# Kernel tuning notes

Measured on AMD Instinct MI355X. Metric: run time of the kernel, lower is better.

## Reference

```python
import jax, jax.numpy as jnp
import numpy as np

NEG_INF = -1e9  # stands in for the -inf diagonal mask of criss-cross attention
BN_EPS = 1e-5


def conv1x1(x, w, b=None):
    # x: [B,Cin,H,W], w: [Cout,Cin]
    y = jnp.einsum('bchw,oc->bohw', x, w)
    if b is not None:
        y = y + b[None, :, None, None]
    return y


def criss_cross(qf, kf, vf, q_w, q_b, k_w, k_b, v_w, v_b, gamma):
    # Criss-cross attention (CCNet): row + column affinity, joint softmax, aggregate.
    B, C, H, W = vf.shape
    q = conv1x1(qf, q_w, q_b)  # [B,Ci,H,W]
    k = conv1x1(kf, k_w, k_b)  # [B,Ci,H,W]
    v = conv1x1(vf, v_w, v_b)  # [B,C,H,W]
    # column-wise (along H) energy, with -inf on the self position (h == h')
    eH = jnp.einsum('bchw,bcHw->bhwH', q, k)
    eH = eH + NEG_INF * jnp.eye(H, dtype=eH.dtype)[:, None, :]  # [H,1,H] broadcasts over w
    # row-wise (along W) energy
    eW = jnp.einsum('bchw,bchW->bhwW', q, k)
    att = jax.nn.softmax(jnp.concatenate([eH, eW], axis=-1), axis=-1)  # [B,H,W,H+W]
    aH, aW = att[..., :H], att[..., H:]
    outH = jnp.einsum('bcHw,bhwH->bchw', v, aH)
    outW = jnp.einsum('bchW,bhwW->bchw', v, aW)
    return gamma * (outH + outW) + vf


def batchnorm(x, scale, bias):
    # training-mode BN over (N,H,W)
    mean = x.mean(axis=(0, 2, 3), keepdims=True)
    var = x.var(axis=(0, 2, 3), keepdims=True)
    xh = (x - mean) * jax.lax.rsqrt(var + BN_EPS)
    return xh * scale[None, :, None, None] + bias[None, :, None, None]


def setup_inputs() -> dict:
    key = jax.random.key(0)
    ks = jax.random.split(key, 16)
    B, C, H, W = 8, 512, 96, 96
    Hh, Wh = 48, 48
    Cin = C // 2    # 256
    Ci = C // 16    # 32
    s = 0.02
    inp = {
        'low_feature': jax.random.normal(ks[0], (B, C, H, W), jnp.float32),
        'high_feature': jax.random.normal(ks[1], (B, C, Hh, Wh), jnp.float32),
        'conv1_w': jax.random.normal(ks[2], (Cin, C), jnp.float32) * s,
        'conv1_b': jnp.zeros((Cin,), jnp.float32),
        'conv2_w': jax.random.normal(ks[3], (Cin, C), jnp.float32) * s,
        'conv2_b': jnp.zeros((Cin,), jnp.float32),
        'q_w': jax.random.normal(ks[4], (Ci, Cin), jnp.float32) * s,
        'q_b': jnp.zeros((Ci,), jnp.float32),
        'k_w': jax.random.normal(ks[5], (Ci, Cin), jnp.float32) * s,
        'k_b': jnp.zeros((Ci,), jnp.float32),
        'v_w': jax.random.normal(ks[6], (Cin, Cin), jnp.float32) * s,
        'v_b': jnp.zeros((Cin,), jnp.float32),
        'gamma': jnp.array(0.1, jnp.float32),
        'bottleneck_w': jax.random.normal(ks[7], (C, Cin + C), jnp.float32) * s,
        'bn_scale': jnp.ones((C,), jnp.float32),
        'bn_bias': jnp.zeros((C,), jnp.float32),
    }
    return inp


def reference(low_feature, high_feature, conv1_w, conv1_b, conv2_w, conv2_b,
              q_w, q_b, k_w, k_b, v_w, v_b, gamma, bottleneck_w, bn_scale, bn_bias):
    B, C, H, W = low_feature.shape
    hf = jax.image.resize(high_feature, (B, high_feature.shape[1], H, W), method='bilinear')
    qf = conv1x1(low_feature, conv1_w, conv1_b)   # [B,C/2,H,W]
    vf = conv1x1(hf, conv2_w, conv2_b)            # [B,C/2,H,W]
    for _ in range(2):  # module applies the same attention twice
        vf = criss_cross(qf, vf, vf, q_w, q_b, k_w, k_b, v_w, v_b, gamma)
    cat = jnp.concatenate([vf, hf], axis=1)       # [B, C/2 + C, H, W]
    out = conv1x1(cat, bottleneck_w)              # bias=False
    out = batchnorm(out, bn_scale, bn_bias)
    return jax.nn.relu(out)
```

## Files before the change

### kernel.cpp

```cpp
#include <hip/hip_runtime.h>
#include <hip/hip_bf16.h>

typedef __hip_bfloat16 bf16;
typedef __attribute__((ext_vector_type(8))) short short8;
typedef __attribute__((ext_vector_type(4))) float f32x4;

constexpr int kHW = 96 * 96;

__device__ __forceinline__ float b2f(bf16 x){ return __bfloat162float(x); }
__device__ __forceinline__ bf16  f2b(float x){ return __float2bfloat16(x); }
__device__ __forceinline__ unsigned short b2u(bf16 x){ return *(unsigned short*)&x; }


__global__ void k_zero(float* __restrict__ p){
  int i = blockIdx.x*256 + threadIdx.x;
  if (i < 1024) p[i] = 0.0f;
}

__global__ void k_cvt(const float* __restrict__ s, bf16* __restrict__ d, int n){
  int i = blockIdx.x*256 + threadIdx.x;
  if (i < n) d[i] = f2b(s[i]);
}

__global__ __launch_bounds__(256) void k_upsample(const float* __restrict__ hi,
                                                  bf16* __restrict__ hf_t){
  int y = blockIdx.x, b = blockIdx.y, t = threadIdx.x;
  int j = y >> 1;
  int j0, j1; float wy0, wy1;
  if ((y & 1) == 0){ j0 = j - 1; if (j0 < 0) j0 = 0; j1 = j; wy0 = 0.25f; wy1 = 0.75f; }
  else             { j0 = j; j1 = j + 1; if (j1 > 47) j1 = 47; wy0 = 0.75f; wy1 = 0.25f; }
  __shared__ __align__(16) float sm[2][128][49];
  for (int c0 = 0; c0 < 512; c0 += 128){
    for (int e = t; e < 2*128*48; e += 256){
      int cl = e / 96; int r = e % 96; int jj = r / 48; int i = r % 48;
      int row = jj ? j1 : j0;
      sm[jj][cl][i] = hi[(((size_t)b*512 + c0 + cl)*48 + row)*48 + i];
    }
    __syncthreads();
    for (int e = t; e < 96*128; e += 256){
      int x = e >> 7; int cl = e & 127;
      int i = x >> 1; int i0, i1; float wx0, wx1;
      if ((x & 1) == 0){ i0 = i - 1; if (i0 < 0) i0 = 0; i1 = i; wx0 = 0.25f; wx1 = 0.75f; }
      else             { i0 = i; i1 = i + 1; if (i1 > 47) i1 = 47; wx0 = 0.75f; wx1 = 0.25f; }
      float v = wy0*(wx0*sm[0][cl][i0] + wx1*sm[0][cl][i1])
              + wy1*(wx0*sm[1][cl][i0] + wx1*sm[1][cl][i1]);
      hf_t[(((size_t)b*96 + x)*96 + y)*512 + c0 + cl] = f2b(v);
    }
    __syncthreads();
  }
}

__global__ void k_qqw(const float* __restrict__ q_w, const float* __restrict__ c1_w,
                      bf16* __restrict__ qq_wb){
  int gid = blockIdx.x*256 + threadIdx.x;
  int o = gid >> 9, c = gid & 511;
  float acc = 0.f;
  for (int k = 0; k < 256; k++) acc += q_w[o*256 + k] * c1_w[k*512 + c];
  qq_wb[gid] = f2b(acc);
}
__global__ void k_qqb(const float* __restrict__ q_w, const float* __restrict__ c1_b,
                      const float* __restrict__ q_b, float* __restrict__ qq_b){
  int o = threadIdx.x; if (o >= 32) return;
  float acc = q_b[o];
  for (int k = 0; k < 256; k++) acc += q_w[o*256 + k] * c1_b[k];
  qq_b[o] = acc;
}

__global__ __launch_bounds__(256) void k_mfma_gemm(const bf16* __restrict__ A,
                                                   const bf16* __restrict__ Wb,
                                                   const float* __restrict__ bias,
                                                   bf16* __restrict__ out,
                                                   int K, int O){
  int b = blockIdx.z, n0 = blockIdx.x*128, o0 = blockIdx.y*128;
  int t = threadIdx.x, lane = t & 63, wv = t >> 6;
  int m_off = (wv & 1)*64, o_off = (wv >> 1)*64;
  int lm = lane & 15, lk = lane >> 4;
  __shared__ __align__(16) bf16 As[2][128*40];
  __shared__ __align__(16) bf16 Ws[2][128*40];
  f32x4 acc[4][4] = {};
  const bf16* Ab = A + (size_t)b*kHW*K;
  int nl0 = t >> 2, p0 = (t & 3)*8;
  uint4 pa0, pa1, pw0, pw1;
  pa0 = *(const uint4*)&Ab[(size_t)(n0+nl0)*K + p0];
  pa1 = *(const uint4*)&Ab[(size_t)(n0+nl0+64)*K + p0];
  pw0 = *(const uint4*)&Wb[(size_t)(o0+nl0)*K + p0];
  pw1 = *(const uint4*)&Wb[(size_t)(o0+nl0+64)*K + p0];
  *(uint4*)&As[0][nl0*40 + p0]      = pa0;
  *(uint4*)&As[0][(nl0+64)*40 + p0] = pa1;
  *(uint4*)&Ws[0][nl0*40 + p0]      = pw0;
  *(uint4*)&Ws[0][(nl0+64)*40 + p0] = pw1;
  int cur = 0;
  int NS = K >> 5;
  for (int s = 0; s < NS; s++){
    if (s+1 < NS){
      int c0 = (s+1)*32;
      pa0 = *(const uint4*)&Ab[(size_t)(n0+nl0)*K + c0 + p0];
      pa1 = *(const uint4*)&Ab[(size_t)(n0+nl0+64)*K + c0 + p0];
      pw0 = *(const uint4*)&Wb[(size_t)(o0+nl0)*K + c0 + p0];
      pw1 = *(const uint4*)&Wb[(size_t)(o0+nl0+64)*K + c0 + p0];
    }
    __syncthreads();
    short8 af[4], bfr[4];
    #pragma unroll
    for (int i = 0; i < 4; i++){
      af[i]  = *(const short8*)&As[cur][(m_off + i*16 + lm)*40 + lk*8];
      bfr[i] = *(const short8*)&Ws[cur][(o_off + i*16 + lm)*40 + lk*8];
    }
    #pragma unroll
    for (int i = 0; i < 4; i++)
      #pragma unroll
      for (int j = 0; j < 4; j++)
        acc[i][j] = __builtin_amdgcn_mfma_f32_16x16x32_bf16(af[i], bfr[j], acc[i][j], 0, 0, 0);
    if (s+1 < NS){
      int nx = cur ^ 1;
      *(uint4*)&As[nx][nl0*40 + p0]      = pa0;
      *(uint4*)&As[nx][(nl0+64)*40 + p0] = pa1;
      *(uint4*)&Ws[nx][nl0*40 + p0]      = pw0;
      *(uint4*)&Ws[nx][(nl0+64)*40 + p0] = pw1;
      cur = nx;
    }
  }
  #pragma unroll
  for (int j = 0; j < 4; j++){
    int oc = o0 + o_off + j*16 + lm;
    float bs = bias ? bias[oc] : 0.0f;
    #pragma unroll
    for (int i = 0; i < 4; i++){
      int rbase = n0 + m_off + i*16 + lk*4;
      #pragma unroll
      for (int r = 0; r < 4; r++)
        out[((size_t)b*kHW + rbase + r)*(size_t)O + oc] = f2b(acc[i][j][r] + bs);
    }
  }
}

__global__ __launch_bounds__(256) void k_bneck_mfma(const bf16* __restrict__ vf,
                                                    const bf16* __restrict__ hf,
                                                    const bf16* __restrict__ Wb,
                                                    bf16* __restrict__ out,
                                                    float* __restrict__ s1,
                                                    float* __restrict__ s2){
  int b = blockIdx.z, n0 = blockIdx.x*128, o0 = blockIdx.y*128;
  int t = threadIdx.x, lane = t & 63, wv = t >> 6;
  int m_off = (wv & 1)*64, o_off = (wv >> 1)*64;
  int lm = lane & 15, lk = lane >> 4;
  __shared__ __align__(16) bf16 As[2][128*40];
  __shared__ __align__(16) bf16 Ws[2][128*40];
  __shared__ float l1[128];
  __shared__ float l2[128];
  if (t < 128){ l1[t] = 0.f; l2[t] = 0.f; }
  f32x4 acc[4][4] = {};
  int nl0 = t >> 2, p0 = (t & 3)*8;
  const bf16* vfb = vf + (size_t)b*kHW*256;
  const bf16* hfb = hf + (size_t)b*kHW*512;
  uint4 pa0, pa1, pw0, pw1;
  pa0 = *(const uint4*)&vfb[(size_t)(n0+nl0)*256 + p0];
  pa1 = *(const uint4*)&vfb[(size_t)(n0+nl0+64)*256 + p0];
  pw0 = *(const uint4*)&Wb[(size_t)(o0+nl0)*768 + p0];
  pw1 = *(const uint4*)&Wb[(size_t)(o0+nl0+64)*768 + p0];
  *(uint4*)&As[0][nl0*40 + p0]      = pa0;
  *(uint4*)&As[0][(nl0+64)*40 + p0] = pa1;
  *(uint4*)&Ws[0][nl0*40 + p0]      = pw0;
  *(uint4*)&Ws[0][(nl0+64)*40 + p0] = pw1;
  int cur = 0;
  for (int s = 0; s < 24; s++){
    if (s+1 < 24){
      int c0 = (s+1)*32;
      if (c0 < 256){
        pa0 = *(const uint4*)&vfb[(size_t)(n0+nl0)*256 + c0 + p0];
        pa1 = *(const uint4*)&vfb[(size_t)(n0+nl0+64)*256 + c0 + p0];
      } else {
        int cc = c0 - 256;
        pa0 = *(const uint4*)&hfb[(size_t)(n0+nl0)*512 + cc + p0];
        pa1 = *(const uint4*)&hfb[(size_t)(n0+nl0+64)*512 + cc + p0];
      }
      pw0 = *(const uint4*)&Wb[(size_t)(o0+nl0)*768 + c0 + p0];
      pw1 = *(const uint4*)&Wb[(size_t)(o0+nl0+64)*768 + c0 + p0];
    }
    __syncthreads();
    short8 af[4], bfr[4];
    #pragma unroll
    for (int i = 0; i < 4; i++){
      af[i]  = *(const short8*)&As[cur][(m_off + i*16 + lm)*40 + lk*8];
      bfr[i] = *(const short8*)&Ws[cur][(o_off + i*16 + lm)*40 + lk*8];
    }
    #pragma unroll
    for (int i = 0; i < 4; i++)
      #pragma unroll
      for (int j = 0; j < 4; j++)
        acc[i][j] = __builtin_amdgcn_mfma_f32_16x16x32_bf16(af[i], bfr[j], acc[i][j], 0, 0, 0);
    if (s+1 < 24){
      int nx = cur ^ 1;
      *(uint4*)&As[nx][nl0*40 + p0]      = pa0;
      *(uint4*)&As[nx][(nl0+64)*40 + p0] = pa1;
      *(uint4*)&Ws[nx][nl0*40 + p0]      = pw0;
      *(uint4*)&Ws[nx][(nl0+64)*40 + p0] = pw1;
      cur = nx;
    }
  }
  #pragma unroll
  for (int j = 0; j < 4; j++){
    int oc = o0 + o_off + j*16 + lm;
    float p1 = 0.f, p2 = 0.f;
    #pragma unroll
    for (int i = 0; i < 4; i++){
      int rbase = n0 + m_off + i*16 + lk*4;
      #pragma unroll
      for (int r = 0; r < 4; r++){
        float v = acc[i][j][r];
        p1 += v; p2 += v*v;
        out[((size_t)b*kHW + rbase + r)*512 + oc] = f2b(v);
      }
    }
    int cl = o_off + j*16 + lm;
    atomicAdd(&l1[cl], p1);
    atomicAdd(&l2[cl], p2);
  }
  __syncthreads();
  if (t < 128){
    atomicAdd(&s1[o0 + t], l1[t]);
    atomicAdd(&s2[o0 + t], l2[t]);
  }
}

__global__ __launch_bounds__(256) void k_qmfma(const float* __restrict__ low,
                                               const bf16* __restrict__ qq_wb,
                                               const float* __restrict__ qq_b,
                                               bf16* __restrict__ q_t){
  int n0 = blockIdx.x*64, b = blockIdx.y, t = threadIdx.x;
  int lane = t & 63, wv = t >> 6;
  int m_off = wv*16;
  int lm = lane & 15, lk = lane >> 4;
  __shared__ __align__(16) bf16 As[64*36];
  __shared__ __align__(16) bf16 Ws[32*40];
  f32x4 acc[2] = {};
  const float* low_b = low + (size_t)b*512*kHW;
  int c2 = (t & 15)*2;
  int xg = t >> 4;
  for (int c0 = 0; c0 < 512; c0 += 32){
    const float* p0 = low_b + (size_t)(c0 + c2)*kHW + n0 + xg*4;
    float4 a0 = *(const float4*)p0;
    float4 a1 = *(const float4*)(p0 + kHW);
    float f0[4] = {a0.x, a0.y, a0.z, a0.w};
    float f1[4] = {a1.x, a1.y, a1.z, a1.w};
    #pragma unroll
    for (int u = 0; u < 4; u++){
      ushort2 pr;
      bf16 v0 = f2b(f0[u]), v1 = f2b(f1[u]);
      pr.x = b2u(v0); pr.y = b2u(v1);
      *(ushort2*)&As[(xg*4 + u)*36 + c2] = pr;
    }
    if (t < 128){
      int ol = t >> 2, p = t & 3;
      *(uint4*)&Ws[ol*40 + p*8] = *(const uint4*)&qq_wb[(size_t)ol*512 + c0 + p*8];
    }
    __syncthreads();
    short8 af = *(const short8*)&As[(m_off + lm)*36 + lk*8];
    short8 b0 = *(const short8*)&Ws[lm*40 + lk*8];
    short8 b1 = *(const short8*)&Ws[(16 + lm)*40 + lk*8];
    acc[0] = __builtin_amdgcn_mfma_f32_16x16x32_bf16(af, b0, acc[0], 0, 0, 0);
    acc[1] = __builtin_amdgcn_mfma_f32_16x16x32_bf16(af, b1, acc[1], 0, 0, 0);
    __syncthreads();
  }
  #pragma unroll
  for (int j = 0; j < 2; j++){
    int oc = j*16 + lm;
    float bs = qq_b[oc];
    #pragma unroll
    for (int r = 0; r < 4; r++){
      int ng = n0 + m_off + lk*4 + r;
      int h = ng / 96, x = ng - h*96;
      q_t[(((size_t)b*96 + x)*96 + h)*32 + oc] = f2b(acc[j][r] + bs);
    }
  }
}

template<int BN, int OT>
__global__ __launch_bounds__(256) void k_gemm_bb(const bf16* __restrict__ A,
                                                 const float* __restrict__ Wt,
                                                 const float* __restrict__ bias,
                                                 bf16* __restrict__ out,
                                                 int Cin, int O){
  constexpr int TN = BN/4;
  int b = blockIdx.z, n0 = blockIdx.x*BN, o0 = blockIdx.y*OT, t = threadIdx.x;
  int tn = t % TN, to = t / TN;
  __shared__ __align__(16) float As[32][BN+4];
  __shared__ __align__(16) float Ws[32][OT+4];
  float acc[4][4] = {};
  const bf16* Ab = A + (size_t)b*kHW*Cin;
  for (int c0 = 0; c0 < Cin; c0 += 32){
    for (int e = t; e < BN*32; e += 256){
      int nl = e >> 5, kk = e & 31;
      As[kk][nl] = b2f(Ab[(size_t)(n0+nl)*Cin + c0 + kk]);
    }
    for (int e = t; e < OT*32; e += 256){
      int ol = e >> 5, kk = e & 31;
      Ws[kk][ol] = Wt[(size_t)(o0+ol)*Cin + c0 + kk];
    }
    __syncthreads();
    #pragma unroll
    for (int kk = 0; kk < 32; kk++){
      float4 av = *(const float4*)&As[kk][tn*4];
      float4 wv = *(const float4*)&Ws[kk][to*4];
      float a_[4] = {av.x, av.y, av.z, av.w};
      float w_[4] = {wv.x, wv.y, wv.z, wv.w};
      #pragma unroll
      for (int i = 0; i < 4; i++)
        #pragma unroll
        for (int jj = 0; jj < 4; jj++) acc[i][jj] += a_[i]*w_[jj];
    }
    __syncthreads();
  }
  #pragma unroll
  for (int i = 0; i < 4; i++){
    size_t base = ((size_t)b*kHW + n0 + tn*4 + i)*(size_t)O + o0 + to*4;
    #pragma unroll
    for (int jj = 0; jj < 4; jj++) out[base + jj] = f2b(acc[i][jj] + bias[o0 + to*4 + jj]);
  }
}

__global__ __launch_bounds__(256) void k_eH(const bf16* __restrict__ q_t,
                                            const bf16* __restrict__ k_t,
                                            bf16* __restrict__ att){
  int w = blockIdx.x, b = blockIdx.y, t = threadIdx.x;
  __shared__ float Qs[96][33];
  __shared__ float Ks[96][33];
  const bf16* Qp = q_t + (((size_t)b*96 + w)*96)*32;
  const bf16* Kp = k_t + (((size_t)b*96 + w)*96)*32;
  for (int e = t; e < 3072; e += 256){ Qs[e>>5][e&31] = b2f(Qp[e]); Ks[e>>5][e&31] = b2f(Kp[e]); }
  __syncthreads();
  int tj = t % 16, th = t / 16;
  float acc[6][6] = {};
  #pragma unroll 4
  for (int c = 0; c < 32; c++){
    float qa[6], kb[6];
    #pragma unroll
    for (int i = 0; i < 6; i++) qa[i] = Qs[th*6 + i][c];
    #pragma unroll
    for (int jj = 0; jj < 6; jj++) kb[jj] = Ks[tj*6 + jj][c];
    #pragma unroll
    for (int i = 0; i < 6; i++)
      #pragma unroll
      for (int jj = 0; jj < 6; jj++) acc[i][jj] += qa[i]*kb[jj];
  }
  #pragma unroll
  for (int i = 0; i < 6; i++){
    int h = th*6 + i;
    size_t base = (((size_t)b*96 + h)*96 + w)*192;
    #pragma unroll
    for (int jj = 0; jj < 6; jj++){
      int jg = tj*6 + jj;
      float e = acc[i][jj];
      if (jg == h) e += -1000000000.0f;
      att[base + jg] = f2b(e);
    }
  }
}

__global__ __launch_bounds__(256) void k_eW(const bf16* __restrict__ q_t,
                                            const bf16* __restrict__ k_t,
                                            bf16* __restrict__ att){
  int h = blockIdx.x, b = blockIdx.y, t = threadIdx.x;
  __shared__ float Qs[96][33];
  __shared__ float Ks[96][33];
  for (int e = t; e < 3072; e += 256){
    int wl = e >> 5, c = e & 31;
    size_t idx = (((size_t)b*96 + wl)*96 + h)*32 + c;
    Qs[wl][c] = b2f(q_t[idx]);
    Ks[wl][c] = b2f(k_t[idx]);
  }
  __syncthreads();
  int tj = t % 16, tw = t / 16;
  float acc[6][6] = {};
  #pragma unroll 4
  for (int c = 0; c < 32; c++){
    float qa[6], kb[6];
    #pragma unroll
    for (int i = 0; i < 6; i++) qa[i] = Qs[tw*6 + i][c];
    #pragma unroll
    for (int jj = 0; jj < 6; jj++) kb[jj] = Ks[tj*6 + jj][c];
    #pragma unroll
    for (int i = 0; i < 6; i++)
      #pragma unroll
      for (int jj = 0; jj < 6; jj++) acc[i][jj] += qa[i]*kb[jj];
  }
  #pragma unroll
  for (int i = 0; i < 6; i++){
    int wl = tw*6 + i;
    size_t base = (((size_t)b*96 + h)*96 + wl)*192 + 96;
    #pragma unroll
    for (int jj = 0; jj < 6; jj++) att[base + tj*6 + jj] = f2b(acc[i][jj]);
  }
}

__global__ __launch_bounds__(256) void k_softmax(bf16* __restrict__ att){
  int t = threadIdx.x;
  int row = blockIdx.x*4 + (t >> 6);
  int lane = t & 63;
  size_t base = (size_t)row * 192;
  float x0 = b2f(att[base + lane]);
  float x1 = b2f(att[base + 64 + lane]);
  float x2 = b2f(att[base + 128 + lane]);
  float m = fmaxf(x0, fmaxf(x1, x2));
  #pragma unroll
  for (int off = 32; off; off >>= 1) m = fmaxf(m, __shfl_xor(m, off));
  float e0 = __expf(x0 - m), e1 = __expf(x1 - m), e2 = __expf(x2 - m);
  float s = e0 + e1 + e2;
  #pragma unroll
  for (int off = 32; off; off >>= 1) s += __shfl_xor(s, off);
  float inv = 1.0f / s;
  att[base + lane]       = f2b(e0 * inv);
  att[base + 64 + lane]  = f2b(e1 * inv);
  att[base + 128 + lane] = f2b(e2 * inv);
}

__global__ __launch_bounds__(256) void k_outH_mfma(const bf16* __restrict__ att,
                                                   const bf16* __restrict__ v_t,
                                                   bf16* __restrict__ accb){
  int w = blockIdx.x, b = blockIdx.y, t = threadIdx.x;
  int lane = t & 63, wv = t >> 6;
  int m_off = (wv & 1)*48, o_off = (wv >> 1)*128;
  int lm = lane & 15, lk = lane >> 4;
  __shared__ __align__(16) bf16 As[96*36];
  __shared__ __align__(16) bf16 Vt[256*36];
  f32x4 acc[3][8] = {};
  const bf16* Vb = v_t + ((size_t)b*96 + w)*96*256;
  for (int j0 = 0; j0 < 96; j0 += 32){
    for (int e = t; e < 384; e += 256){
      int h = e >> 2, p = e & 3;
      *(uint4*)&As[h*36 + p*8] =
        *(const uint4*)&att[(((size_t)b*96 + h)*96 + w)*192 + j0 + p*8];
    }
    for (int e = t; e < 512; e += 256){
      int jj2 = (e & 15)*2, cg = e >> 4;
      const bf16* p = Vb + (size_t)(j0 + jj2)*256 + cg*8;
      uint4 a0 = *(const uint4*)p;
      uint4 a1 = *(const uint4*)(p + 256);
      const unsigned short* u0 = (const unsigned short*)&a0;
      const unsigned short* u1 = (const unsigned short*)&a1;
      #pragma unroll
      for (int u = 0; u < 8; u++){
        ushort2 pr; pr.x = u0[u]; pr.y = u1[u];
        *(ushort2*)&Vt[(cg*8 + u)*36 + jj2] = pr;
      }
    }
    __syncthreads();
    short8 af[3], bfr[8];
    #pragma unroll
    for (int i = 0; i < 3; i++)
      af[i] = *(const short8*)&As[(m_off + i*16 + lm)*36 + lk*8];
    #pragma unroll
    for (int j = 0; j < 8; j++)
      bfr[j] = *(const short8*)&Vt[(o_off + j*16 + lm)*36 + lk*8];
    #pragma unroll
    for (int i = 0; i < 3; i++)
      #pragma unroll
      for (int j = 0; j < 8; j++)
        acc[i][j] = __builtin_amdgcn_mfma_f32_16x16x32_bf16(af[i], bfr[j], acc[i][j], 0, 0, 0);
    __syncthreads();
  }
  #pragma unroll
  for (int j = 0; j < 8; j++){
    int c = o_off + j*16 + lm;
    #pragma unroll
    for (int i = 0; i < 3; i++){
      int hbase = m_off + i*16 + lk*4;
      #pragma unroll
      for (int r = 0; r < 4; r++)
        accb[(((size_t)b*96 + w)*96 + hbase + r)*256 + c] = f2b(acc[i][j][r]);
    }
  }
}

__global__ __launch_bounds__(256) void k_outW_mfma(const bf16* __restrict__ att,
                                                   const bf16* __restrict__ v_t,
                                                   const bf16* __restrict__ accb,
                                                   const float* __restrict__ gamma_p,
                                                   bf16* __restrict__ vf_t){
  int h = blockIdx.x, b = blockIdx.y, t = threadIdx.x;
  int lane = t & 63, wv = t >> 6;
  int m_off = (wv & 1)*48, o_off = (wv >> 1)*128;
  int lm = lane & 15, lk = lane >> 4;
  __shared__ __align__(16) bf16 As[96*36];
  __shared__ __align__(16) bf16 Vt[256*36];
  f32x4 acc[3][8] = {};
  for (int j0 = 0; j0 < 96; j0 += 32){
    for (int e = t; e < 384; e += 256){
      int wl = e >> 2, p = e & 3;
      *(uint4*)&As[wl*36 + p*8] =
        *(const uint4*)&att[(((size_t)b*96 + h)*96 + wl)*192 + 96 + j0 + p*8];
    }
    for (int e = t; e < 512; e += 256){
      int jj2 = (e & 15)*2, cg = e >> 4;
      const bf16* p = v_t + (((size_t)b*96 + j0 + jj2)*96 + h)*256 + cg*8;
      uint4 a0 = *(const uint4*)p;
      uint4 a1 = *(const uint4*)(p + 96*256);
      const unsigned short* u0 = (const unsigned short*)&a0;
      const unsigned short* u1 = (const unsigned short*)&a1;
      #pragma unroll
      for (int u = 0; u < 8; u++){
        ushort2 pr; pr.x = u0[u]; pr.y = u1[u];
        *(ushort2*)&Vt[(cg*8 + u)*36 + jj2] = pr;
      }
    }
    __syncthreads();
    short8 af[3], bfr[8];
    #pragma unroll
    for (int i = 0; i < 3; i++)
      af[i] = *(const short8*)&As[(m_off + i*16 + lm)*36 + lk*8];
    #pragma unroll
    for (int j = 0; j < 8; j++)
      bfr[j] = *(const short8*)&Vt[(o_off + j*16 + lm)*36 + lk*8];
    #pragma unroll
    for (int i = 0; i < 3; i++)
      #pragma unroll
      for (int j = 0; j < 8; j++)
        acc[i][j] = __builtin_amdgcn_mfma_f32_16x16x32_bf16(af[i], bfr[j], acc[i][j], 0, 0, 0);
    __syncthreads();
  }
  float g = gamma_p[0];
  #pragma unroll
  for (int j = 0; j < 8; j++){
    int c = o_off + j*16 + lm;
    #pragma unroll
    for (int i = 0; i < 3; i++){
      int wbase = m_off + i*16 + lk*4;
      #pragma unroll
      for (int r = 0; r < 4; r++){
        size_t idx = (((size_t)b*96 + wbase + r)*96 + h)*256 + c;
        vf_t[idx] = f2b(b2f(vf_t[idx]) + g*(acc[i][j][r] + b2f(accb[idx])));
      }
    }
  }
}

__global__ void k_bnprep(const float* __restrict__ s1, const float* __restrict__ s2,
                         const float* __restrict__ sc, const float* __restrict__ bi,
                         float2* __restrict__ ab){
  int co = blockIdx.x*256 + threadIdx.x;
  if (co >= 512) return;
  const float N = 73728.0f;
  float mean = s1[co] / N;
  float var  = s2[co] / N - mean*mean;
  if (var < 0.f) var = 0.f;
  float a = rsqrtf(var + 1e-5f) * sc[co];
  ab[co] = make_float2(a, bi[co] - mean*a);
}

__global__ __launch_bounds__(256) void k_bnout(const bf16* __restrict__ bt,
                                               const float2* __restrict__ ab,
                                               float* __restrict__ out){
  int w0 = blockIdx.x*32, h = blockIdx.y, b = blockIdx.z, t = threadIdx.x;
  __shared__ float Tl[32][33];
  for (int co0 = 0; co0 < 512; co0 += 32){
    for (int e = t; e < 1024; e += 256){
      int wl = e >> 5, co = e & 31;
      Tl[wl][co] = b2f(bt[(((size_t)b*96 + w0 + wl)*96 + h)*512 + co0 + co]);
    }
    __syncthreads();
    for (int e = t; e < 1024; e += 256){
      int co = e >> 5, wl = e & 31;
      float2 s = ab[co0 + co];
      float v = fmaxf(Tl[wl][co]*s.x + s.y, 0.0f);
      out[(((size_t)b*512 + co0 + co)*96 + h)*96 + w0 + wl] = v;
    }
    __syncthreads();
  }
}

extern "C" void kernel_launch(void* const* d_in, const int* in_sizes, int n_in,
                              void* d_out, int out_size, void* d_ws, size_t ws_size,
                              hipStream_t stream){
  (void)in_sizes; (void)n_in; (void)out_size; (void)ws_size;
  const float* low   = (const float*)d_in[0];
  const float* high  = (const float*)d_in[1];
  const float* c1w   = (const float*)d_in[2];
  const float* c1b   = (const float*)d_in[3];
  const float* c2w   = (const float*)d_in[4];
  const float* c2b   = (const float*)d_in[5];
  const float* qw    = (const float*)d_in[6];
  const float* qb    = (const float*)d_in[7];
  const float* kw    = (const float*)d_in[8];
  const float* kb    = (const float*)d_in[9];
  const float* vw    = (const float*)d_in[10];
  const float* vb    = (const float*)d_in[11];
  const float* gamma = (const float*)d_in[12];
  const float* bw    = (const float*)d_in[13];
  const float* bns   = (const float*)d_in[14];
  const float* bnb   = (const float*)d_in[15];
  float* out = (float*)d_out;

  char* wsb = (char*)d_ws;
  bf16*   hf_t = (bf16*) (wsb + 0);
  bf16*   vf_t = (bf16*) (wsb + 75497472);
  bf16*   q_t  = (bf16*) (wsb + 113246208);
  bf16*   qq_wb= (bf16*) (wsb + 117964800);
  float*  qq_b = (float*)(wsb + 118030336);
  float*  s1   = (float*)(wsb + 118030464);
  float*  s2   = (float*)(wsb + 118032512);
  float2* ab   = (float2*)(wsb + 118034560);
  bf16*   wbb  = (bf16*) (wsb + 118038656);
  bf16*   wc2  = (bf16*) (wsb + 118825088);
  bf16*   wv   = (bf16*) (wsb + 119087232);
  bf16*   v_t  = (bf16*) (wsb + 119218304);
  bf16*   att  = (bf16*) (wsb + 156967040);
  bf16*   accb = (bf16*) (wsb + 185278592);
  bf16*   k_t  = (bf16*) (wsb + 185278592);
  bf16*   bt   = (bf16*) (wsb + 119218304);

  k_zero<<<4, 256, 0, stream>>>(s1);
  k_cvt<<<1536, 256, 0, stream>>>(bw,  wbb, 393216);
  k_cvt<<<512,  256, 0, stream>>>(c2w, wc2, 131072);
  k_cvt<<<256,  256, 0, stream>>>(vw,  wv,  65536);
  k_upsample<<<dim3(96, 8), 256, 0, stream>>>(high, hf_t);
  k_qqw<<<64, 256, 0, stream>>>(qw, c1w, qq_wb);
  k_qqb<<<1, 64, 0, stream>>>(qw, c1b, qb, qq_b);
  k_mfma_gemm<<<dim3(72, 2, 8), 256, 0, stream>>>(hf_t, wc2, c2b, vf_t, 512, 256);
  k_qmfma<<<dim3(144, 8), 256, 0, stream>>>(low, qq_wb, qq_b, q_t);

  for (int r = 0; r < 2; r++){
    k_gemm_bb<128, 32><<<dim3(72, 1, 8), 256, 0, stream>>>(vf_t, kw, kb, k_t, 256, 32);
    k_mfma_gemm<<<dim3(72, 2, 8), 256, 0, stream>>>(vf_t, wv, vb, v_t, 256, 256);
    k_eH<<<dim3(96, 8), 256, 0, stream>>>(q_t, k_t, att);
    k_eW<<<dim3(96, 8), 256, 0, stream>>>(q_t, k_t, att);
    k_softmax<<<18432, 256, 0, stream>>>(att);
    k_outH_mfma<<<dim3(96, 8), 256, 0, stream>>>(att, v_t, accb);
    k_outW_mfma<<<dim3(96, 8), 256, 0, stream>>>(att, v_t, accb, gamma, vf_t);
  }

  k_bneck_mfma<<<dim3(72, 4, 8), 256, 0, stream>>>(vf_t, hf_t, wbb, bt, s1, s2);
  k_bnprep<<<2, 256, 0, stream>>>(s1, s2, bns, bnb, ab);
  k_bnout<<<dim3(3, 96, 8), 256, 0, stream>>>(bt, ab, out);
}
```

Before: 1.014 ms.

## Use MFMA for key projection and XOR-swizzle shared tiles in GEMMs

```diff
diff --git a/kernel.cpp b/kernel.cpp
--- a/kernel.cpp
+++ b/kernel.cpp
@@ -10,6 +10,8 @@
 __device__ __forceinline__ float b2f(bf16 x){ return __bfloat162float(x); }
 __device__ __forceinline__ bf16  f2b(float x){ return __float2bfloat16(x); }
 __device__ __forceinline__ unsigned short b2u(bf16 x){ return *(unsigned short*)&x; }
+
+#define SW(r, g) ((r)*32 + ((((g) ^ (((r) >> 1) & 3))) << 3))
 
 
 __global__ void k_zero(float* __restrict__ p){
@@ -75,20 +77,20 @@
   int t = threadIdx.x, lane = t & 63, wv = t >> 6;
   int m_off = (wv & 1)*64, o_off = (wv >> 1)*64;
   int lm = lane & 15, lk = lane >> 4;
-  __shared__ __align__(16) bf16 As[2][128*40];
-  __shared__ __align__(16) bf16 Ws[2][128*40];
+  __shared__ __align__(16) bf16 As[2][128*32];
+  __shared__ __align__(16) bf16 Ws[2][128*32];
   f32x4 acc[4][4] = {};
   const bf16* Ab = A + (size_t)b*kHW*K;
-  int nl0 = t >> 2, p0 = (t & 3)*8;
+  int nl0 = t >> 2, gp = t & 3, p0 = gp*8;
   uint4 pa0, pa1, pw0, pw1;
   pa0 = *(const uint4*)&Ab[(size_t)(n0+nl0)*K + p0];
   pa1 = *(const uint4*)&Ab[(size_t)(n0+nl0+64)*K + p0];
   pw0 = *(const uint4*)&Wb[(size_t)(o0+nl0)*K + p0];
   pw1 = *(const uint4*)&Wb[(size_t)(o0+nl0+64)*K + p0];
-  *(uint4*)&As[0][nl0*40 + p0]      = pa0;
-  *(uint4*)&As[0][(nl0+64)*40 + p0] = pa1;
-  *(uint4*)&Ws[0][nl0*40 + p0]      = pw0;
-  *(uint4*)&Ws[0][(nl0+64)*40 + p0] = pw1;
+  *(uint4*)&As[0][SW(nl0, gp)]    = pa0;
+  *(uint4*)&As[0][SW(nl0+64, gp)] = pa1;
+  *(uint4*)&Ws[0][SW(nl0, gp)]    = pw0;
+  *(uint4*)&Ws[0][SW(nl0+64, gp)] = pw1;
   int cur = 0;
   int NS = K >> 5;
   for (int s = 0; s < NS; s++){
@@ -103,8 +105,8 @@
     short8 af[4], bfr[4];
     #pragma unroll
     for (int i = 0; i < 4; i++){
-      af[i]  = *(const short8*)&As[cur][(m_off + i*16 + lm)*40 + lk*8];
-      bfr[i] = *(const short8*)&Ws[cur][(o_off + i*16 + lm)*40 + lk*8];
+      af[i]  = *(const short8*)&As[cur][SW(m_off + i*16 + lm, lk)];
+      bfr[i] = *(const short8*)&Ws[cur][SW(o_off + i*16 + lm, lk)];
     }
     #pragma unroll
     for (int i = 0; i < 4; i++)
@@ -113,10 +115,10 @@
         acc[i][j] = __builtin_amdgcn_mfma_f32_16x16x32_bf16(af[i], bfr[j], acc[i][j], 0, 0, 0);
     if (s+1 < NS){
       int nx = cur ^ 1;
-      *(uint4*)&As[nx][nl0*40 + p0]      = pa0;
-      *(uint4*)&As[nx][(nl0+64)*40 + p0] = pa1;
-      *(uint4*)&Ws[nx][nl0*40 + p0]      = pw0;
-      *(uint4*)&Ws[nx][(nl0+64)*40 + p0] = pw1;
+      *(uint4*)&As[nx][SW(nl0, gp)]    = pa0;
+      *(uint4*)&As[nx][SW(nl0+64, gp)] = pa1;
+      *(uint4*)&Ws[nx][SW(nl0, gp)]    = pw0;
+      *(uint4*)&Ws[nx][SW(nl0+64, gp)] = pw1;
       cur = nx;
     }
   }
@@ -144,13 +146,13 @@
   int t = threadIdx.x, lane = t & 63, wv = t >> 6;
   int m_off = (wv & 1)*64, o_off = (wv >> 1)*64;
   int lm = lane & 15, lk = lane >> 4;
-  __shared__ __align__(16) bf16 As[2][128*40];
-  __shared__ __align__(16) bf16 Ws[2][128*40];
+  __shared__ __align__(16) bf16 As[2][128*32];
+  __shared__ __align__(16) bf16 Ws[2][128*32];
   __shared__ float l1[128];
   __shared__ float l2[128];
   if (t < 128){ l1[t] = 0.f; l2[t] = 0.f; }
   f32x4 acc[4][4] = {};
-  int nl0 = t >> 2, p0 = (t & 3)*8;
+  int nl0 = t >> 2, gp = t & 3, p0 = gp*8;
   const bf16* vfb = vf + (size_t)b*kHW*256;
   const bf16* hfb = hf + (size_t)b*kHW*512;
   uint4 pa0, pa1, pw0, pw1;
@@ -158,10 +160,10 @@
   pa1 = *(const uint4*)&vfb[(size_t)(n0+nl0+64)*256 + p0];
   pw0 = *(const uint4*)&Wb[(size_t)(o0+nl0)*768 + p0];
   pw1 = *(const uint4*)&Wb[(size_t)(o0+nl0+64)*768 + p0];
-  *(uint4*)&As[0][nl0*40 + p0]      = pa0;
-  *(uint4*)&As[0][(nl0+64)*40 + p0] = pa1;
-  *(uint4*)&Ws[0][nl0*40 + p0]      = pw0;
-  *(uint4*)&Ws[0][(nl0+64)*40 + p0] = pw1;
+  *(uint4*)&As[0][SW(nl0, gp)]    = pa0;
+  *(uint4*)&As[0][SW(nl0+64, gp)] = pa1;
+  *(uint4*)&Ws[0][SW(nl0, gp)]    = pw0;
+  *(uint4*)&Ws[0][SW(nl0+64, gp)] = pw1;
   int cur = 0;
   for (int s = 0; s < 24; s++){
     if (s+1 < 24){
@@ -181,8 +183,8 @@
     short8 af[4], bfr[4];
     #pragma unroll
     for (int i = 0; i < 4; i++){
-      af[i]  = *(const short8*)&As[cur][(m_off + i*16 + lm)*40 + lk*8];
-      bfr[i] = *(const short8*)&Ws[cur][(o_off + i*16 + lm)*40 + lk*8];
+      af[i]  = *(const short8*)&As[cur][SW(m_off + i*16 + lm, lk)];
+      bfr[i] = *(const short8*)&Ws[cur][SW(o_off + i*16 + lm, lk)];
     }
     #pragma unroll
     for (int i = 0; i < 4; i++)
@@ -191,10 +193,10 @@
         acc[i][j] = __builtin_amdgcn_mfma_f32_16x16x32_bf16(af[i], bfr[j], acc[i][j], 0, 0, 0);
     if (s+1 < 24){
       int nx = cur ^ 1;
-      *(uint4*)&As[nx][nl0*40 + p0]      = pa0;
-      *(uint4*)&As[nx][(nl0+64)*40 + p0] = pa1;
-      *(uint4*)&Ws[nx][nl0*40 + p0]      = pw0;
-      *(uint4*)&Ws[nx][(nl0+64)*40 + p0] = pw1;
+      *(uint4*)&As[nx][SW(nl0, gp)]    = pa0;
+      *(uint4*)&As[nx][SW(nl0+64, gp)] = pa1;
+      *(uint4*)&Ws[nx][SW(nl0, gp)]    = pw0;
+      *(uint4*)&Ws[nx][SW(nl0+64, gp)] = pw1;
       cur = nx;
     }
   }
@@ -275,47 +277,67 @@
   }
 }
 
-template<int BN, int OT>
-__global__ __launch_bounds__(256) void k_gemm_bb(const bf16* __restrict__ A,
-                                                 const float* __restrict__ Wt,
-                                                 const float* __restrict__ bias,
-                                                 bf16* __restrict__ out,
-                                                 int Cin, int O){
-  constexpr int TN = BN/4;
-  int b = blockIdx.z, n0 = blockIdx.x*BN, o0 = blockIdx.y*OT, t = threadIdx.x;
-  int tn = t % TN, to = t / TN;
-  __shared__ __align__(16) float As[32][BN+4];
-  __shared__ __align__(16) float Ws[32][OT+4];
-  float acc[4][4] = {};
-  const bf16* Ab = A + (size_t)b*kHW*Cin;
-  for (int c0 = 0; c0 < Cin; c0 += 32){
-    for (int e = t; e < BN*32; e += 256){
-      int nl = e >> 5, kk = e & 31;
-      As[kk][nl] = b2f(Ab[(size_t)(n0+nl)*Cin + c0 + kk]);
-    }
-    for (int e = t; e < OT*32; e += 256){
-      int ol = e >> 5, kk = e & 31;
-      Ws[kk][ol] = Wt[(size_t)(o0+ol)*Cin + c0 + kk];
-    }
-    __syncthreads();
-    #pragma unroll
-    for (int kk = 0; kk < 32; kk++){
-      float4 av = *(const float4*)&As[kk][tn*4];
-      float4 wv = *(const float4*)&Ws[kk][to*4];
-      float a_[4] = {av.x, av.y, av.z, av.w};
-      float w_[4] = {wv.x, wv.y, wv.z, wv.w};
-      #pragma unroll
-      for (int i = 0; i < 4; i++)
-        #pragma unroll
-        for (int jj = 0; jj < 4; jj++) acc[i][jj] += a_[i]*w_[jj];
-    }
-    __syncthreads();
-  }
-  #pragma unroll
-  for (int i = 0; i < 4; i++){
-    size_t base = ((size_t)b*kHW + n0 + tn*4 + i)*(size_t)O + o0 + to*4;
-    #pragma unroll
-    for (int jj = 0; jj < 4; jj++) out[base + jj] = f2b(acc[i][jj] + bias[o0 + to*4 + jj]);
+__global__ __launch_bounds__(256) void k_kmfma(const bf16* __restrict__ A,
+                                               const bf16* __restrict__ Wk,
+                                               const float* __restrict__ bias,
+                                               bf16* __restrict__ out){
+  int n0 = blockIdx.x*128, b = blockIdx.y;
+  int t = threadIdx.x, lane = t & 63, wv = t >> 6;
+  int m_off = wv*32;
+  int lm = lane & 15, lk = lane >> 4;
+  __shared__ __align__(16) bf16 As[2][128*32];
+  __shared__ __align__(16) bf16 Ws[2][32*32];
+  f32x4 acc[2][2] = {};
+  const bf16* Ab = A + (size_t)b*kHW*256;
+  int nl0 = t >> 2, gp = t & 3, p0 = gp*8;
+  int ol = t >> 2;
+  uint4 pa0, pa1, pw;
+  pa0 = *(const uint4*)&Ab[(size_t)(n0+nl0)*256 + p0];
+  pa1 = *(const uint4*)&Ab[(size_t)(n0+nl0+64)*256 + p0];
+  if (t < 128) pw = *(const uint4*)&Wk[(size_t)ol*256 + p0];
+  *(uint4*)&As[0][SW(nl0, gp)]    = pa0;
+  *(uint4*)&As[0][SW(nl0+64, gp)] = pa1;
+  if (t < 128) *(uint4*)&Ws[0][SW(ol, gp)] = pw;
+  int cur = 0;
+  for (int s = 0; s < 8; s++){
+    if (s+1 < 8){
+      int c0 = (s+1)*32;
+      pa0 = *(const uint4*)&Ab[(size_t)(n0+nl0)*256 + c0 + p0];
+      pa1 = *(const uint4*)&Ab[(size_t)(n0+nl0+64)*256 + c0 + p0];
+      if (t < 128) pw = *(const uint4*)&Wk[(size_t)ol*256 + c0 + p0];
+    }
+    __syncthreads();
+    short8 af[2], bfr[2];
+    #pragma unroll
+    for (int i = 0; i < 2; i++)
+      af[i] = *(const short8*)&As[cur][SW(m_off + i*16 + lm, lk)];
+    #pragma unroll
+    for (int j = 0; j < 2; j++)
+      bfr[j] = *(const short8*)&Ws[cur][SW(j*16 + lm, lk)];
+    #pragma unroll
+    for (int i = 0; i < 2; i++)
+      #pragma unroll
+      for (int j = 0; j < 2; j++)
+        acc[i][j] = __builtin_amdgcn_mfma_f32_16x16x32_bf16(af[i], bfr[j], acc[i][j], 0, 0, 0);
+    if (s+1 < 8){
+      int nx = cur ^ 1;
+      *(uint4*)&As[nx][SW(nl0, gp)]    = pa0;
+      *(uint4*)&As[nx][SW(nl0+64, gp)] = pa1;
+      if (t < 128) *(uint4*)&Ws[nx][SW(ol, gp)] = pw;
+      cur = nx;
+    }
+  }
+  #pragma unroll
+  for (int j = 0; j < 2; j++){
+    int oc = j*16 + lm;
+    float bs = bias[oc];
+    #pragma unroll
+    for (int i = 0; i < 2; i++){
+      int rbase = n0 + m_off + i*16 + lk*4;
+      #pragma unroll
+      for (int r = 0; r < 4; r++)
+        out[((size_t)b*kHW + rbase + r)*32 + oc] = f2b(acc[i][j][r] + bs);
+    }
   }
 }
 
@@ -595,6 +617,7 @@
   bf16*   vf_t = (bf16*) (wsb + 75497472);
   bf16*   q_t  = (bf16*) (wsb + 113246208);
   bf16*   qq_wb= (bf16*) (wsb + 117964800);
+  bf16*   wk   = (bf16*) (wsb + 117997568);
   float*  qq_b = (float*)(wsb + 118030336);
   float*  s1   = (float*)(wsb + 118030464);
   float*  s2   = (float*)(wsb + 118032512);
@@ -612,6 +635,7 @@
   k_cvt<<<1536, 256, 0, stream>>>(bw,  wbb, 393216);
   k_cvt<<<512,  256, 0, stream>>>(c2w, wc2, 131072);
   k_cvt<<<256,  256, 0, stream>>>(vw,  wv,  65536);
+  k_cvt<<<32,   256, 0, stream>>>(kw,  wk,  8192);
   k_upsample<<<dim3(96, 8), 256, 0, stream>>>(high, hf_t);
   k_qqw<<<64, 256, 0, stream>>>(qw, c1w, qq_wb);
   k_qqb<<<1, 64, 0, stream>>>(qw, c1b, qb, qq_b);
@@ -619,7 +643,7 @@
   k_qmfma<<<dim3(144, 8), 256, 0, stream>>>(low, qq_wb, qq_b, q_t);
 
   for (int r = 0; r < 2; r++){
-    k_gemm_bb<128, 32><<<dim3(72, 1, 8), 256, 0, stream>>>(vf_t, kw, kb, k_t, 256, 32);
+    k_kmfma<<<dim3(72, 8), 256, 0, stream>>>(vf_t, wk, kb, k_t);
     k_mfma_gemm<<<dim3(72, 2, 8), 256, 0, stream>>>(vf_t, wv, vb, v_t, 256, 256);
     k_eH<<<dim3(96, 8), 256, 0, stream>>>(q_t, k_t, att);
     k_eW<<<dim3(96, 8), 256, 0, stream>>>(q_t, k_t, att);
```

New measurement: 956.3 us. 1.06x faster.
